# Kernel tuning notes

Measured on AMD Instinct MI355X. Metric: run time of the kernel, lower is better.

## Reference

```python
import jax, jax.numpy as jnp
import numpy as np

DIM, HEADS, K = 128, 4, 7
HD = DIM // HEADS


def _nbr_idx(n, k):
    # NATTEN boundary-clamped neighborhood (dilation=1): window start clamped to [0, n-k]
    i = np.arange(n)
    start = np.clip(i - k // 2, 0, n - k)
    idx = start[:, None] + np.arange(k)[None, :]          # (n, k) absolute neighbor index
    rel = idx - i[:, None] + (k - 1)                      # (n, k) index into 2k-1 rpb axis
    return jnp.asarray(idx), jnp.asarray(rel)


def _ln(x, w, b, eps=1e-5):
    mu = jnp.mean(x, -1, keepdims=True)
    var = jnp.var(x, -1, keepdims=True)
    return (x - mu) * jax.lax.rsqrt(var + eps) * w + b


def setup_inputs() -> dict:
    key = jax.random.key(0)
    ks = jax.random.split(key, 16)
    B, H, W, C = 1, 128, 128, DIM
    f = jax.random.normal
    inp = {
        'x': f(ks[0], (B, H, W, C), jnp.float32),
        'y': f(ks[1], (B, H, W, C), jnp.float32),
        'qv_w': f(ks[2], (2 * C, C), jnp.float32) * 0.02,
        'qv_b': jnp.zeros((2 * C,), jnp.float32),
        'k_w': f(ks[3], (C, C), jnp.float32) * 0.02,
        'k_b': jnp.zeros((C,), jnp.float32),
        'rpb': f(ks[4], (HEADS, 2 * K - 1, 2 * K - 1), jnp.float32) * 0.02,
        'proj_w': f(ks[5], (C, C), jnp.float32) * 0.02,
        'proj_b': jnp.zeros((C,), jnp.float32),
        'n1_w': jnp.ones((C,), jnp.float32),
        'n1_b': jnp.zeros((C,), jnp.float32),
        'n2_w': jnp.ones((C,), jnp.float32),
        'n2_b': jnp.zeros((C,), jnp.float32),
        'fc1_w': f(ks[6], (4 * C, C), jnp.float32) * 0.02,
        'fc1_b': jnp.zeros((4 * C,), jnp.float32),
        'fc2_w': f(ks[7], (C, 4 * C), jnp.float32) * 0.02,
        'fc2_b': jnp.zeros((C,), jnp.float32),
    }
    return inp


def _block(x, y, qv_w, qv_b, k_w, k_b, rpb, proj_w, proj_b,
           n1_w, n1_b, n2_w, n2_b, fc1_w, fc1_b, fc2_w, fc2_b):
    B, H, W, C = x.shape
    scale = HD ** -0.5
    # ---- CrossNat2D attention on norm1(x) vs y ----
    xn = _ln(x, n1_w, n1_b)
    qv = xn @ qv_w.T + qv_b                               # (B,H,W,2C)
    q = qv[..., :C].reshape(B, H, W, HEADS, HD) * scale
    v = qv[..., C:].reshape(B, H, W, HEADS, HD)
    k = (y @ k_w.T + k_b).reshape(B, H, W, HEADS, HD)

    idx_h, rel_h = _nbr_idx(H, K)
    idx_w, rel_w = _nbr_idx(W, K)
    # gather neighborhoods: (B, H, K, W, K, HEADS, HD)
    k_nbr = k[:, idx_h][:, :, :, idx_w]
    v_nbr = v[:, idx_h][:, :, :, idx_w]

    # attention logits over KxK neighborhood
    attn = jnp.einsum('bijhd,biajchd->bijhac', q, k_nbr)  # (B,H,W,heads,K,K)
    bias = rpb[:, rel_h][..., rel_w]                      # (heads,H,K,W,K)
    attn = attn + jnp.transpose(bias, (1, 3, 0, 2, 4))    # broadcast over B
    attn = jax.nn.softmax(attn.reshape(B, H, W, HEADS, K * K), axis=-1)
    attn = attn.reshape(B, H, W, HEADS, K, K)

    out = jnp.einsum('bijhac,biajchd->bijhd', attn, v_nbr).reshape(B, H, W, C)
    out = out @ proj_w.T + proj_b

    x = x + out
    # ---- MLP ----
    h = _ln(x, n2_w, n2_b) @ fc1_w.T + fc1_b
    h = jax.nn.gelu(h, approximate=False) @ fc2_w.T + fc2_b
    return x + h


def reference(x, y, qv_w, qv_b, k_w, k_b, rpb, proj_w, proj_b,
              n1_w, n1_b, n2_w, n2_b, fc1_w, fc1_b, fc2_w, fc2_b):
    return _block(x, y, qv_w, qv_b, k_w, k_b, rpb, proj_w, proj_b,
                  n1_w, n1_b, n2_w, n2_b, fc1_w, fc1_b, fc2_w, fc2_b)
```

## Files before the change

kernel.cpp:

```cpp
#include <hip/hip_runtime.h>
#include <hip/hip_bf16.h>


#define N_PIX 16384
#define C 128
#define HEADS 4
#define HD 32
#define HW 128

typedef __hip_bfloat16 bf16;
typedef __attribute__((ext_vector_type(8))) short bf16x8;
typedef __attribute__((ext_vector_type(4))) float f32x4;

union U32x4 { unsigned int u[4]; bf16x8 b; };

__device__ __forceinline__ short f2bs(float f) {
    bf16 h = __float2bfloat16(f);
    return (short)__bfloat16_as_ushort(h);
}
__device__ __forceinline__ float bs2f(short s) {
    __hip_bfloat16_raw r; r.x = (unsigned short)s;
    return __bfloat162float(__hip_bfloat16(r));
}
__device__ __forceinline__ float gelu_f(float v) {
    const float z = 1.5957691216f * (v + 0.044715f * v * v * v);
    return v / (1.f + __expf(-z));
}
__device__ __forceinline__ unsigned int pack2(float a, float b) {
    return (unsigned int)(unsigned short)f2bs(a) |
           ((unsigned int)(unsigned short)f2bs(b) << 16);
}

__global__ __launch_bounds__(256) void k_wconv(
    const float* __restrict__ qv_w, const float* __restrict__ k_w,
    const float* __restrict__ proj_w, const float* __restrict__ fc1_w,
    const float* __restrict__ fc2_w,
    short* __restrict__ wqv, short* __restrict__ wk, short* __restrict__ wproj,
    short* __restrict__ wfc1, short* __restrict__ wfc2) {
    const int i = blockIdx.x * 256 + threadIdx.x;
    if (i < 32768) wqv[i] = f2bs(qv_w[i]);
    if (i < 16384) { wk[i] = f2bs(k_w[i]); wproj[i] = f2bs(proj_w[i]); }
    if (i < 65536) { wfc1[i] = f2bs(fc1_w[i]); wfc2[i] = f2bs(fc2_w[i]); }
}

__global__ __launch_bounds__(256, 4) void k_qkv(
    const float* __restrict__ x, const float* __restrict__ y,
    const short* __restrict__ wqv, const float* __restrict__ qv_b,
    const short* __restrict__ wk, const float* __restrict__ k_b,
    const float* __restrict__ n1_w, const float* __restrict__ n1_b,
    bf16* __restrict__ qb, bf16* __restrict__ vb, bf16* __restrict__ kb) {
    __shared__ float xr[16][132];
    __shared__ short xn[16][136];
    __shared__ short yl[16][136];
    __shared__ float muA[16], riA[16];
    const int t = threadIdx.x;
    const int pix0 = (blockIdx.x & 7) * 2048 + (blockIdx.x >> 3) * 16;
    for (int e = t; e < 512; e += 256) {
        const int r = e >> 5, c4 = (e & 31) * 4;
        const float4 xv = *(const float4*)(x + (size_t)(pix0 + r) * C + c4);
        *(float4*)&xr[r][c4] = xv;
        const float4 yv = *(const float4*)(y + (size_t)(pix0 + r) * C + c4);
        uint2 yp; yp.x = pack2(yv.x, yv.y); yp.y = pack2(yv.z, yv.w);
        *(uint2*)&yl[r][c4] = yp;
    }
    __syncthreads();
    if (t < 128) {
        const int r = t >> 3, s = t & 7;
        float sm = 0.f, sq = 0.f;
        for (int i = 0; i < 16; i++) { float v = xr[r][s * 16 + i]; sm += v; sq += v * v; }
        for (int m = 1; m < 8; m <<= 1) { sm += __shfl_xor(sm, m, 64); sq += __shfl_xor(sq, m, 64); }
        if (s == 0) {
            const float mu = sm * (1.f / 128.f);
            const float var = sq * (1.f / 128.f) - mu * mu;
            muA[r] = mu; riA[r] = rsqrtf(var + 1e-5f);
        }
    }
    __syncthreads();
    for (int e = t; e < 2048; e += 256) {
        const int r = e >> 7, c = e & 127;
        xn[r][c] = f2bs((xr[r][c] - muA[r]) * riA[r] * n1_w[c] + n1_b[c]);
    }
    __syncthreads();
    const int wave = t >> 6, lane = t & 63, quad = lane >> 4, l15 = lane & 15;
    const float scale = 0.1767766952966369f;
    {
        bf16x8 aA[4];
#pragma unroll
        for (int kt = 0; kt < 4; kt++)
            aA[kt] = *(const bf16x8*)&xn[l15][kt * 32 + quad * 8];
#pragma unroll
        for (int s = 0; s < 4; s++) {
            const int n = (wave * 4 + s) * 16 + l15;
            f32x4 acc = {0.f, 0.f, 0.f, 0.f};
#pragma unroll
            for (int kt = 0; kt < 4; kt++) {
                bf16x8 b = *(const bf16x8*)&wqv[n * C + kt * 32 + quad * 8];
                acc = __builtin_amdgcn_mfma_f32_16x16x32_bf16(aA[kt], b, acc, 0, 0, 0);
            }
            const float bias = qv_b[n];
#pragma unroll
            for (int r = 0; r < 4; r++) {
                const int m = quad * 4 + r;
                const float v = acc[r] + bias;
                if (n < C) qb[(size_t)(pix0 + m) * C + n] = __float2bfloat16(v * scale);
                else       vb[(size_t)(pix0 + m) * C + (n - C)] = __float2bfloat16(v);
            }
        }
    }
    {
        bf16x8 aY[4];
#pragma unroll
        for (int kt = 0; kt < 4; kt++)
            aY[kt] = *(const bf16x8*)&yl[l15][kt * 32 + quad * 8];
        const int n0 = (wave * 2) * 16 + l15, n1 = (wave * 2 + 1) * 16 + l15;
        f32x4 a0 = {0.f, 0.f, 0.f, 0.f}, a1 = {0.f, 0.f, 0.f, 0.f};
#pragma unroll
        for (int kt = 0; kt < 4; kt++) {
            bf16x8 b0 = *(const bf16x8*)&wk[n0 * C + kt * 32 + quad * 8];
            bf16x8 b1 = *(const bf16x8*)&wk[n1 * C + kt * 32 + quad * 8];
            a0 = __builtin_amdgcn_mfma_f32_16x16x32_bf16(aY[kt], b0, a0, 0, 0, 0);
            a1 = __builtin_amdgcn_mfma_f32_16x16x32_bf16(aY[kt], b1, a1, 0, 0, 0);
        }
        const float b0s = k_b[n0], b1s = k_b[n1];
#pragma unroll
        for (int r = 0; r < 4; r++) {
            const int m = quad * 4 + r;
            kb[(size_t)(pix0 + m) * C + n0] = __float2bfloat16(a0[r] + b0s);
            kb[(size_t)(pix0 + m) * C + n1] = __float2bfloat16(a1[r] + b1s);
        }
    }
}

__global__ __launch_bounds__(256, 4) void k_fam(
    const bf16* __restrict__ qb, const bf16* __restrict__ kb,
    const bf16* __restrict__ vb, const float* __restrict__ rpb,
    const float* __restrict__ x,
    const short* __restrict__ wproj, const float* __restrict__ proj_b,
    const float* __restrict__ n2_w, const float* __restrict__ n2_b,
    const short* __restrict__ wfc1, const float* __restrict__ fc1_b,
    const short* __restrict__ wfc2, const float* __restrict__ fc2_b,
    float* __restrict__ out) {
    __shared__ short U[14784];
    __shared__ float muA[16], riA[16];
    short* const aoL = U;
    short* const x1b = U + 2176;
    short* const xnb = U + 4288;
    short* const hb  = U + 6464;
    const int t = threadIdx.x;
    const int wave = t >> 6, lane = t & 63, quad = lane >> 4, l15 = lane & 15;
    const int h = wave;
    const int tile = (blockIdx.x & 7) * 128 + (blockIdx.x >> 3);
    const int i0 = (tile >> 5) * 4, j0 = (tile & 31) * 4;
    const int rs = min(max(i0 - 3, 0), 118);
    const int cs = min(max(j0 - 3, 0), 118);
    const int pA = (i0 + (l15 >> 2)) * HW + j0 + (l15 & 3);
    const bf16x8 aQ = *(const bf16x8*)(qb + (size_t)pA * C + h * HD + quad * 8);
    const int nR0 = h * 16 + l15, nR1 = (h + 4) * 16 + l15;
    float xres0[4], xres1[4];
#pragma unroll
    for (int r = 0; r < 4; r++) {
        const int m = quad * 4 + r;
        const int p = (i0 + (m >> 2)) * HW + j0 + (m & 3);
        xres0[r] = x[(size_t)p * C + nR0];
        xres1[r] = x[(size_t)p * C + nR1];
    }
    uint4 vst[7];
#pragma unroll
    for (int it = 0; it < 7; ++it) {
        const int u = t + it * 256;
        const int r = u >> 4, seg = u & 15;
        const int sr = min(r, 99);
        const size_t g = (size_t)((rs + sr / 10) * HW + cs + sr % 10) * C + seg * 8;
        *(uint4*)&U[r * 132 + seg * 8] = *(const uint4*)(kb + g);
        vst[it] = *(const uint4*)(vb + g);
    }
    __syncthreads();
    f32x4 S[7];
#pragma unroll
    for (int nt = 0; nt < 7; nt++) {
        const bf16x8 bK = *(const bf16x8*)&U[(nt * 16 + l15) * 132 + h * HD + quad * 8];
        f32x4 z = {0.f, 0.f, 0.f, 0.f};
        S[nt] = __builtin_amdgcn_mfma_f32_16x16x32_bf16(bK, aQ, z, 0, 0, 0);
    }
    __syncthreads();
#pragma unroll
    for (int it = 0; it < 7; ++it) {
        const int u = t + it * 256;
        const int r = u >> 4, seg = u & 15;
        *(uint4*)&U[r * 132 + seg * 8] = vst[it];
    }
    const float* rpbh = rpb + h * 169;
    const int ii = i0 + (l15 >> 2), jj0_ = j0 + (l15 & 3);
    const int shi = min(max(ii - 3, 0), 121);
    const int swj = min(max(jj0_ - 3, 0), 121);
    float best = -1e30f;
#pragma unroll
    for (int nt = 0; nt < 7; nt++) {
#pragma unroll
        for (int r = 0; r < 4; r++) {
            const int nb = nt * 16 + quad * 4 + r;
            const int ai = rs + nb / 10, aj = cs + nb % 10;
            const bool valid = (nb < 100) & (ai >= shi) & (ai <= shi + 6) & (aj >= swj) & (aj <= swj + 6);
            const int ri = min(max(ai - ii + 6, 0), 12);
            const int rj = min(max(aj - jj0_ + 6, 0), 12);
            const float v = valid ? (S[nt][r] + rpbh[ri * 13 + rj]) : -1e30f;
            S[nt][r] = v;
            best = fmaxf(best, v);
        }
    }
    best = fmaxf(best, __shfl_xor(best, 16, 64));
    best = fmaxf(best, __shfl_xor(best, 32, 64));
    float s = 0.f;
#pragma unroll
    for (int nt = 0; nt < 7; nt++) {
#pragma unroll
        for (int r = 0; r < 4; r++) {
            const float e = __expf(S[nt][r] - best);
            S[nt][r] = e;
            s += e;
        }
    }
    s += __shfl_xor(s, 16, 64);
    s += __shfl_xor(s, 32, 64);
    const float smx = 1.f / s;
    unsigned int pk[14];
#pragma unroll
    for (int nt = 0; nt < 7; nt++) {
        pk[nt * 2]     = pack2(S[nt][0] * smx, S[nt][1] * smx);
        pk[nt * 2 + 1] = pack2(S[nt][2] * smx, S[nt][3] * smx);
    }
    __syncthreads();
    f32x4 O0 = {0.f, 0.f, 0.f, 0.f}, O1 = {0.f, 0.f, 0.f, 0.f};
#pragma unroll
    for (int kt = 0; kt < 3; kt++) {
        U32x4 uu;
#pragma unroll
        for (int w = 0; w < 4; w++) {
            const int qs = ((quad & 1) << 1) + (w >> 1);
            const int src = (qs << 4) | l15;
            const unsigned va = __shfl(pk[4 * kt + (w & 1)], src, 64);
            const unsigned vb2 = __shfl(pk[4 * kt + 2 + (w & 1)], src, 64);
            uu.u[w] = (quad >> 1) ? vb2 : va;
        }
        const bf16x8 aP = uu.b;
#pragma unroll
        for (int nt2 = 0; nt2 < 2; nt2++) {
            const int ch = h * HD + nt2 * 16 + l15;
            const int base = (kt * 32 + quad * 8) * 132 + ch;
            bf16x8 bV;
#pragma unroll
            for (int jj = 0; jj < 8; jj++) bV[jj] = U[base + jj * 132];
            if (nt2 == 0) O0 = __builtin_amdgcn_mfma_f32_16x16x32_bf16(aP, bV, O0, 0, 0, 0);
            else          O1 = __builtin_amdgcn_mfma_f32_16x16x32_bf16(aP, bV, O1, 0, 0, 0);
        }
    }
    {
        U32x4 uu;
#pragma unroll
        for (int w = 0; w < 4; w++) {
            const int qs = ((quad & 1) << 1) + (w >> 1);
            const int src = (qs << 4) | l15;
            const unsigned va = __shfl(pk[12 + (w & 1)], src, 64);
            uu.u[w] = (quad >> 1) ? 0u : va;
        }
        const bf16x8 aP = uu.b;
#pragma unroll
        for (int nt2 = 0; nt2 < 2; nt2++) {
            const int ch = h * HD + nt2 * 16 + l15;
            bf16x8 bV = {0, 0, 0, 0, 0, 0, 0, 0};
            if (quad < 2) {
                const int base = (96 + quad * 8) * 132 + ch;
#pragma unroll
                for (int jj = 0; jj < 8; jj++) bV[jj] = U[base + jj * 132];
            }
            if (nt2 == 0) O0 = __builtin_amdgcn_mfma_f32_16x16x32_bf16(aP, bV, O0, 0, 0, 0);
            else          O1 = __builtin_amdgcn_mfma_f32_16x16x32_bf16(aP, bV, O1, 0, 0, 0);
        }
    }
    __syncthreads();
#pragma unroll
    for (int r = 0; r < 4; r++) {
        const int m = quad * 4 + r;
        aoL[m * 136 + h * HD + l15] = f2bs(O0[r]);
        aoL[m * 136 + h * HD + 16 + l15] = f2bs(O1[r]);
    }
    __syncthreads();
    float x1f0[4], x1f1[4];
    {
        bf16x8 aO[4];
#pragma unroll
        for (int kt = 0; kt < 4; kt++)
            aO[kt] = *(const bf16x8*)&aoL[l15 * 136 + kt * 32 + quad * 8];
        f32x4 a0 = {0.f, 0.f, 0.f, 0.f}, a1 = {0.f, 0.f, 0.f, 0.f};
#pragma unroll
        for (int kt = 0; kt < 4; kt++) {
            bf16x8 b0 = *(const bf16x8*)&wproj[nR0 * C + kt * 32 + quad * 8];
            bf16x8 b1 = *(const bf16x8*)&wproj[nR1 * C + kt * 32 + quad * 8];
            a0 = __builtin_amdgcn_mfma_f32_16x16x32_bf16(aO[kt], b0, a0, 0, 0, 0);
            a1 = __builtin_amdgcn_mfma_f32_16x16x32_bf16(aO[kt], b1, a1, 0, 0, 0);
        }
        const float b0s = proj_b[nR0], b1s = proj_b[nR1];
#pragma unroll
        for (int r = 0; r < 4; r++) {
            const int m = quad * 4 + r;
            const float v0 = xres0[r] + a0[r] + b0s;
            const float v1 = xres1[r] + a1[r] + b1s;
            x1f0[r] = v0; x1f1[r] = v1;
            x1b[m * 132 + nR0] = f2bs(v0);
            x1b[m * 132 + nR1] = f2bs(v1);
        }
    }
    __syncthreads();
    if (t < 128) {
        const int r = t >> 3, s2 = t & 7;
        float sm = 0.f, sq = 0.f;
        for (int i2 = 0; i2 < 16; i2++) { float v = bs2f(x1b[r * 132 + s2 * 16 + i2]); sm += v; sq += v * v; }
        for (int m = 1; m < 8; m <<= 1) { sm += __shfl_xor(sm, m, 64); sq += __shfl_xor(sq, m, 64); }
        if (s2 == 0) {
            const float mu = sm * (1.f / 128.f);
            const float var = sq * (1.f / 128.f) - mu * mu;
            muA[r] = mu; riA[r] = rsqrtf(var + 1e-5f);
        }
    }
    __syncthreads();
    for (int e = t; e < 2048; e += 256) {
        const int r = e >> 7, c = e & 127;
        xnb[r * 136 + c] = f2bs((bs2f(x1b[r * 132 + c]) - muA[r]) * riA[r] * n2_w[c] + n2_b[c]);
    }
    __syncthreads();
    {
        bf16x8 aX[4];
#pragma unroll
        for (int kt = 0; kt < 4; kt++)
            aX[kt] = *(const bf16x8*)&xnb[l15 * 136 + kt * 32 + quad * 8];
#pragma unroll
        for (int a = 0; a < 8; a++) {
            const int n = (wave * 8 + a) * 16 + l15;
            f32x4 acc = {0.f, 0.f, 0.f, 0.f};
#pragma unroll
            for (int kt = 0; kt < 4; kt++) {
                bf16x8 bw = *(const bf16x8*)&wfc1[n * C + kt * 32 + quad * 8];
                acc = __builtin_amdgcn_mfma_f32_16x16x32_bf16(aX[kt], bw, acc, 0, 0, 0);
            }
            const float bias = fc1_b[n];
#pragma unroll
            for (int r = 0; r < 4; r++) {
                const int m = quad * 4 + r;
                hb[m * 520 + n] = f2bs(gelu_f(acc[r] + bias));
            }
        }
    }
    __syncthreads();
    {
        f32x4 a0 = {0.f, 0.f, 0.f, 0.f}, a1 = {0.f, 0.f, 0.f, 0.f};
#pragma unroll
        for (int kt = 0; kt < 16; kt++) {
            const bf16x8 aP = *(const bf16x8*)&hb[l15 * 520 + kt * 32 + quad * 8];
            bf16x8 b0 = *(const bf16x8*)&wfc2[nR0 * 512 + kt * 32 + quad * 8];
            bf16x8 b1 = *(const bf16x8*)&wfc2[nR1 * 512 + kt * 32 + quad * 8];
            a0 = __builtin_amdgcn_mfma_f32_16x16x32_bf16(aP, b0, a0, 0, 0, 0);
            a1 = __builtin_amdgcn_mfma_f32_16x16x32_bf16(aP, b1, a1, 0, 0, 0);
        }
        const float b0s = fc2_b[nR0], b1s = fc2_b[nR1];
#pragma unroll
        for (int r = 0; r < 4; r++) {
            const int m = quad * 4 + r;
            const int p = (i0 + (m >> 2)) * HW + j0 + (m & 3);
            out[(size_t)p * C + nR0] = a0[r] + b0s + x1f0[r];
            out[(size_t)p * C + nR1] = a1[r] + b1s + x1f1[r];
        }
    }
}

extern "C" void kernel_launch(void* const* d_in, const int* in_sizes, int n_in,
                              void* d_out, int out_size, void* d_ws, size_t ws_size,
                              hipStream_t stream) {
    const float* x      = (const float*)d_in[0];
    const float* y      = (const float*)d_in[1];
    const float* qv_w   = (const float*)d_in[2];
    const float* qv_b   = (const float*)d_in[3];
    const float* k_w    = (const float*)d_in[4];
    const float* k_b    = (const float*)d_in[5];
    const float* rpb    = (const float*)d_in[6];
    const float* proj_w = (const float*)d_in[7];
    const float* proj_b = (const float*)d_in[8];
    const float* n1_w   = (const float*)d_in[9];
    const float* n1_b   = (const float*)d_in[10];
    const float* n2_w   = (const float*)d_in[11];
    const float* n2_b   = (const float*)d_in[12];
    const float* fc1_w  = (const float*)d_in[13];
    const float* fc1_b  = (const float*)d_in[14];
    const float* fc2_w  = (const float*)d_in[15];
    const float* fc2_b  = (const float*)d_in[16];
    float* out = (float*)d_out;

    bf16* qb  = (bf16*)d_ws;
    bf16* vb  = qb + (size_t)N_PIX * C;
    bf16* kb  = vb + (size_t)N_PIX * C;
    short* wqv  = (short*)(kb + (size_t)N_PIX * C);
    short* wk   = wqv + 32768;
    short* wproj= wk + 16384;
    short* wfc1 = wproj + 16384;
    short* wfc2 = wfc1 + 65536;

    k_wconv<<<256, 256, 0, stream>>>(qv_w, k_w, proj_w, fc1_w, fc2_w,
                                     wqv, wk, wproj, wfc1, wfc2);
    k_qkv<<<1024, 256, 0, stream>>>(x, y, wqv, qv_b, wk, k_b, n1_w, n1_b,
                                    qb, vb, kb);
    k_fam<<<1024, 256, 0, stream>>>(qb, kb, vb, rpb, x, wproj, proj_b, n2_w, n2_b,
                                    wfc1, fc1_b, wfc2, fc2_b, out);
}
```

Measured before the change: 170.3 us.

## Double threads per block and split attention softmax across two wave groups

Both the QKV and fused attention+MLP kernels move from 256 to 512 threads per block, so each wave owns fewer output columns. In the attention kernel the neighbour tiles are split between two wave groups per head. Their partial max and sum are merged through shared memory, and the probabilities are staged in a new LDS buffer instead of being exchanged by cross-lane shuffles. This is meant to expose more parallel waves and shorten each wave's serial MFMA chain, at the cost of extra barriers, more LDS and a higher occupancy target that may limit registers.

Result: no change. 168.3 us (-1.2%).

```diff
diff --git a/kernel.cpp b/kernel.cpp
--- a/kernel.cpp
+++ b/kernel.cpp
@@ -11,8 +11,6 @@
 typedef __hip_bfloat16 bf16;
 typedef __attribute__((ext_vector_type(8))) short bf16x8;
 typedef __attribute__((ext_vector_type(4))) float f32x4;
-
-union U32x4 { unsigned int u[4]; bf16x8 b; };
 
 __device__ __forceinline__ short f2bs(float f) {
     bf16 h = __float2bfloat16(f);
@@ -43,7 +41,7 @@
     if (i < 65536) { wfc1[i] = f2bs(fc1_w[i]); wfc2[i] = f2bs(fc2_w[i]); }
 }
 
-__global__ __launch_bounds__(256, 4) void k_qkv(
+__global__ __launch_bounds__(512, 8) void k_qkv(
     const float* __restrict__ x, const float* __restrict__ y,
     const short* __restrict__ wqv, const float* __restrict__ qv_b,
     const short* __restrict__ wk, const float* __restrict__ k_b,
@@ -55,8 +53,8 @@
     __shared__ float muA[16], riA[16];
     const int t = threadIdx.x;
     const int pix0 = (blockIdx.x & 7) * 2048 + (blockIdx.x >> 3) * 16;
-    for (int e = t; e < 512; e += 256) {
-        const int r = e >> 5, c4 = (e & 31) * 4;
+    {
+        const int r = t >> 5, c4 = (t & 31) * 4;
         const float4 xv = *(const float4*)(x + (size_t)(pix0 + r) * C + c4);
         *(float4*)&xr[r][c4] = xv;
         const float4 yv = *(const float4*)(y + (size_t)(pix0 + r) * C + c4);
@@ -76,7 +74,7 @@
         }
     }
     __syncthreads();
-    for (int e = t; e < 2048; e += 256) {
+    for (int e = t; e < 2048; e += 512) {
         const int r = e >> 7, c = e & 127;
         xn[r][c] = f2bs((xr[r][c] - muA[r]) * riA[r] * n1_w[c] + n1_b[c]);
     }
@@ -88,23 +86,24 @@
 #pragma unroll
         for (int kt = 0; kt < 4; kt++)
             aA[kt] = *(const bf16x8*)&xn[l15][kt * 32 + quad * 8];
-#pragma unroll
-        for (int s = 0; s < 4; s++) {
-            const int n = (wave * 4 + s) * 16 + l15;
-            f32x4 acc = {0.f, 0.f, 0.f, 0.f};
-#pragma unroll
-            for (int kt = 0; kt < 4; kt++) {
-                bf16x8 b = *(const bf16x8*)&wqv[n * C + kt * 32 + quad * 8];
-                acc = __builtin_amdgcn_mfma_f32_16x16x32_bf16(aA[kt], b, acc, 0, 0, 0);
-            }
-            const float bias = qv_b[n];
-#pragma unroll
-            for (int r = 0; r < 4; r++) {
-                const int m = quad * 4 + r;
-                const float v = acc[r] + bias;
-                if (n < C) qb[(size_t)(pix0 + m) * C + n] = __float2bfloat16(v * scale);
-                else       vb[(size_t)(pix0 + m) * C + (n - C)] = __float2bfloat16(v);
-            }
+        const int n0 = (wave * 2) * 16 + l15, n1 = (wave * 2 + 1) * 16 + l15;
+        f32x4 a0 = {0.f, 0.f, 0.f, 0.f}, a1 = {0.f, 0.f, 0.f, 0.f};
+#pragma unroll
+        for (int kt = 0; kt < 4; kt++) {
+            bf16x8 b0 = *(const bf16x8*)&wqv[n0 * C + kt * 32 + quad * 8];
+            bf16x8 b1 = *(const bf16x8*)&wqv[n1 * C + kt * 32 + quad * 8];
+            a0 = __builtin_amdgcn_mfma_f32_16x16x32_bf16(aA[kt], b0, a0, 0, 0, 0);
+            a1 = __builtin_amdgcn_mfma_f32_16x16x32_bf16(aA[kt], b1, a1, 0, 0, 0);
+        }
+        const float b0s = qv_b[n0], b1s = qv_b[n1];
+#pragma unroll
+        for (int r = 0; r < 4; r++) {
+            const int m = quad * 4 + r;
+            const float v0 = a0[r] + b0s, v1 = a1[r] + b1s;
+            if (n0 < C) qb[(size_t)(pix0 + m) * C + n0] = __float2bfloat16(v0 * scale);
+            else        vb[(size_t)(pix0 + m) * C + (n0 - C)] = __float2bfloat16(v0);
+            if (n1 < C) qb[(size_t)(pix0 + m) * C + n1] = __float2bfloat16(v1 * scale);
+            else        vb[(size_t)(pix0 + m) * C + (n1 - C)] = __float2bfloat16(v1);
         }
     }
     {
@@ -112,26 +111,25 @@
 #pragma unroll
         for (int kt = 0; kt < 4; kt++)
             aY[kt] = *(const bf16x8*)&yl[l15][kt * 32 + quad * 8];
-        const int n0 = (wave * 2) * 16 + l15, n1 = (wave * 2 + 1) * 16 + l15;
+        const int n = wave * 16 + l15;
         f32x4 a0 = {0.f, 0.f, 0.f, 0.f}, a1 = {0.f, 0.f, 0.f, 0.f};
 #pragma unroll
-        for (int kt = 0; kt < 4; kt++) {
-            bf16x8 b0 = *(const bf16x8*)&wk[n0 * C + kt * 32 + quad * 8];
-            bf16x8 b1 = *(const bf16x8*)&wk[n1 * C + kt * 32 + quad * 8];
+        for (int kt = 0; kt < 4; kt += 2) {
+            bf16x8 b0 = *(const bf16x8*)&wk[n * C + kt * 32 + quad * 8];
+            bf16x8 b1 = *(const bf16x8*)&wk[n * C + (kt + 1) * 32 + quad * 8];
             a0 = __builtin_amdgcn_mfma_f32_16x16x32_bf16(aY[kt], b0, a0, 0, 0, 0);
-            a1 = __builtin_amdgcn_mfma_f32_16x16x32_bf16(aY[kt], b1, a1, 0, 0, 0);
-        }
-        const float b0s = k_b[n0], b1s = k_b[n1];
+            a1 = __builtin_amdgcn_mfma_f32_16x16x32_bf16(aY[kt + 1], b1, a1, 0, 0, 0);
+        }
+        const float bs = k_b[n];
 #pragma unroll
         for (int r = 0; r < 4; r++) {
             const int m = quad * 4 + r;
-            kb[(size_t)(pix0 + m) * C + n0] = __float2bfloat16(a0[r] + b0s);
-            kb[(size_t)(pix0 + m) * C + n1] = __float2bfloat16(a1[r] + b1s);
-        }
-    }
-}
-
-__global__ __launch_bounds__(256, 4) void k_fam(
+            kb[(size_t)(pix0 + m) * C + n] = __float2bfloat16(a0[r] + a1[r] + bs);
+        }
+    }
+}
+
+__global__ __launch_bounds__(512, 8) void k_fam(
     const bf16* __restrict__ qb, const bf16* __restrict__ kb,
     const bf16* __restrict__ vb, const float* __restrict__ rpb,
     const float* __restrict__ x,
@@ -141,6 +139,8 @@
     const short* __restrict__ wfc2, const float* __restrict__ fc2_b,
     float* __restrict__ out) {
     __shared__ short U[14784];
+    __shared__ short Pb[16 * 136];
+    __shared__ float pmax[2][4][16], psum[2][4][16];
     __shared__ float muA[16], riA[16];
     short* const aoL = U;
     short* const x1b = U + 2176;
@@ -148,144 +148,125 @@
     short* const hb  = U + 6464;
     const int t = threadIdx.x;
     const int wave = t >> 6, lane = t & 63, quad = lane >> 4, l15 = lane & 15;
-    const int h = wave;
+    const int h = wave & 3, s = wave >> 2;
     const int tile = (blockIdx.x & 7) * 128 + (blockIdx.x >> 3);
     const int i0 = (tile >> 5) * 4, j0 = (tile & 31) * 4;
     const int rs = min(max(i0 - 3, 0), 118);
     const int cs = min(max(j0 - 3, 0), 118);
     const int pA = (i0 + (l15 >> 2)) * HW + j0 + (l15 & 3);
     const bf16x8 aQ = *(const bf16x8*)(qb + (size_t)pA * C + h * HD + quad * 8);
-    const int nR0 = h * 16 + l15, nR1 = (h + 4) * 16 + l15;
-    float xres0[4], xres1[4];
+    const int nW = wave * 16 + l15;
+    float xres[4];
 #pragma unroll
     for (int r = 0; r < 4; r++) {
         const int m = quad * 4 + r;
         const int p = (i0 + (m >> 2)) * HW + j0 + (m & 3);
-        xres0[r] = x[(size_t)p * C + nR0];
-        xres1[r] = x[(size_t)p * C + nR1];
-    }
-    uint4 vst[7];
-#pragma unroll
-    for (int it = 0; it < 7; ++it) {
-        const int u = t + it * 256;
-        const int r = u >> 4, seg = u & 15;
-        const int sr = min(r, 99);
-        const size_t g = (size_t)((rs + sr / 10) * HW + cs + sr % 10) * C + seg * 8;
-        *(uint4*)&U[r * 132 + seg * 8] = *(const uint4*)(kb + g);
-        vst[it] = *(const uint4*)(vb + g);
-    }
-    __syncthreads();
-    f32x4 S[7];
-#pragma unroll
-    for (int nt = 0; nt < 7; nt++) {
-        const bf16x8 bK = *(const bf16x8*)&U[(nt * 16 + l15) * 132 + h * HD + quad * 8];
-        f32x4 z = {0.f, 0.f, 0.f, 0.f};
-        S[nt] = __builtin_amdgcn_mfma_f32_16x16x32_bf16(bK, aQ, z, 0, 0, 0);
-    }
-    __syncthreads();
-#pragma unroll
-    for (int it = 0; it < 7; ++it) {
-        const int u = t + it * 256;
-        const int r = u >> 4, seg = u & 15;
-        *(uint4*)&U[r * 132 + seg * 8] = vst[it];
+        xres[r] = x[(size_t)p * C + nW];
+    }
+    uint4 vst[4];
+#pragma unroll
+    for (int it = 0; it < 4; ++it) {
+        if (it < 3 || t < 256) {
+            const int u = t + it * 512;
+            const int r = u >> 4, seg = u & 15;
+            const int sr = min(r, 99);
+            const size_t g = (size_t)((rs + sr / 10) * HW + cs + sr % 10) * C + seg * 8;
+            *(uint4*)&U[r * 132 + seg * 8] = *(const uint4*)(kb + g);
+            vst[it] = *(const uint4*)(vb + g);
+        }
+    }
+    __syncthreads();
+    f32x4 S[4];
+#pragma unroll
+    for (int ntl = 0; ntl < 4; ntl++) {
+        if (s == 0 || ntl < 3) {
+            const int nt = s * 4 + ntl;
+            const bf16x8 bK = *(const bf16x8*)&U[(nt * 16 + l15) * 132 + h * HD + quad * 8];
+            f32x4 z = {0.f, 0.f, 0.f, 0.f};
+            S[ntl] = __builtin_amdgcn_mfma_f32_16x16x32_bf16(aQ, bK, z, 0, 0, 0);
+        }
+    }
+    __syncthreads();
+#pragma unroll
+    for (int it = 0; it < 4; ++it) {
+        if (it < 3 || t < 256) {
+            const int u = t + it * 512;
+            const int r = u >> 4, seg = u & 15;
+            *(uint4*)&U[r * 132 + seg * 8] = vst[it];
+        }
     }
     const float* rpbh = rpb + h * 169;
-    const int ii = i0 + (l15 >> 2), jj0_ = j0 + (l15 & 3);
-    const int shi = min(max(ii - 3, 0), 121);
-    const int swj = min(max(jj0_ - 3, 0), 121);
-    float best = -1e30f;
-#pragma unroll
-    for (int nt = 0; nt < 7; nt++) {
-#pragma unroll
-        for (int r = 0; r < 4; r++) {
-            const int nb = nt * 16 + quad * 4 + r;
-            const int ai = rs + nb / 10, aj = cs + nb % 10;
-            const bool valid = (nb < 100) & (ai >= shi) & (ai <= shi + 6) & (aj >= swj) & (aj <= swj + 6);
-            const int ri = min(max(ai - ii + 6, 0), 12);
-            const int rj = min(max(aj - jj0_ + 6, 0), 12);
-            const float v = valid ? (S[nt][r] + rpbh[ri * 13 + rj]) : -1e30f;
-            S[nt][r] = v;
-            best = fmaxf(best, v);
-        }
-    }
-    best = fmaxf(best, __shfl_xor(best, 16, 64));
-    best = fmaxf(best, __shfl_xor(best, 32, 64));
-    float s = 0.f;
-#pragma unroll
-    for (int nt = 0; nt < 7; nt++) {
-#pragma unroll
-        for (int r = 0; r < 4; r++) {
-            const float e = __expf(S[nt][r] - best);
-            S[nt][r] = e;
-            s += e;
-        }
-    }
-    s += __shfl_xor(s, 16, 64);
-    s += __shfl_xor(s, 32, 64);
-    const float smx = 1.f / s;
-    unsigned int pk[14];
-#pragma unroll
-    for (int nt = 0; nt < 7; nt++) {
-        pk[nt * 2]     = pack2(S[nt][0] * smx, S[nt][1] * smx);
-        pk[nt * 2 + 1] = pack2(S[nt][2] * smx, S[nt][3] * smx);
-    }
-    __syncthreads();
-    f32x4 O0 = {0.f, 0.f, 0.f, 0.f}, O1 = {0.f, 0.f, 0.f, 0.f};
-#pragma unroll
-    for (int kt = 0; kt < 3; kt++) {
-        U32x4 uu;
-#pragma unroll
-        for (int w = 0; w < 4; w++) {
-            const int qs = ((quad & 1) << 1) + (w >> 1);
-            const int src = (qs << 4) | l15;
-            const unsigned va = __shfl(pk[4 * kt + (w & 1)], src, 64);
-            const unsigned vb2 = __shfl(pk[4 * kt + 2 + (w & 1)], src, 64);
-            uu.u[w] = (quad >> 1) ? vb2 : va;
-        }
-        const bf16x8 aP = uu.b;
-#pragma unroll
-        for (int nt2 = 0; nt2 < 2; nt2++) {
-            const int ch = h * HD + nt2 * 16 + l15;
-            const int base = (kt * 32 + quad * 8) * 132 + ch;
-            bf16x8 bV;
-#pragma unroll
-            for (int jj = 0; jj < 8; jj++) bV[jj] = U[base + jj * 132];
-            if (nt2 == 0) O0 = __builtin_amdgcn_mfma_f32_16x16x32_bf16(aP, bV, O0, 0, 0, 0);
-            else          O1 = __builtin_amdgcn_mfma_f32_16x16x32_bf16(aP, bV, O1, 0, 0, 0);
-        }
-    }
-    {
-        U32x4 uu;
-#pragma unroll
-        for (int w = 0; w < 4; w++) {
-            const int qs = ((quad & 1) << 1) + (w >> 1);
-            const int src = (qs << 4) | l15;
-            const unsigned va = __shfl(pk[12 + (w & 1)], src, 64);
-            uu.u[w] = (quad >> 1) ? 0u : va;
-        }
-        const bf16x8 aP = uu.b;
-#pragma unroll
-        for (int nt2 = 0; nt2 < 2; nt2++) {
-            const int ch = h * HD + nt2 * 16 + l15;
-            bf16x8 bV = {0, 0, 0, 0, 0, 0, 0, 0};
-            if (quad < 2) {
-                const int base = (96 + quad * 8) * 132 + ch;
-#pragma unroll
-                for (int jj = 0; jj < 8; jj++) bV[jj] = U[base + jj * 132];
-            }
-            if (nt2 == 0) O0 = __builtin_amdgcn_mfma_f32_16x16x32_bf16(aP, bV, O0, 0, 0, 0);
-            else          O1 = __builtin_amdgcn_mfma_f32_16x16x32_bf16(aP, bV, O1, 0, 0, 0);
-        }
-    }
-    __syncthreads();
+    float mo[4];
 #pragma unroll
     for (int r = 0; r < 4; r++) {
         const int m = quad * 4 + r;
-        aoL[m * 136 + h * HD + l15] = f2bs(O0[r]);
-        aoL[m * 136 + h * HD + 16 + l15] = f2bs(O1[r]);
-    }
-    __syncthreads();
-    float x1f0[4], x1f1[4];
+        const int ii = i0 + (m >> 2), jj = j0 + (m & 3);
+        const int shi = min(max(ii - 3, 0), 121);
+        const int swj = min(max(jj - 3, 0), 121);
+        float best = -1e30f;
+#pragma unroll
+        for (int ntl = 0; ntl < 4; ntl++) {
+            if (s == 0 || ntl < 3) {
+                const int nb = (s * 4 + ntl) * 16 + l15;
+                const int ai = rs + nb / 10, aj = cs + nb % 10;
+                const bool valid = (nb < 100) & (ai >= shi) & (ai <= shi + 6) & (aj >= swj) & (aj <= swj + 6);
+                const int ri = min(max(ai - ii + 6, 0), 12);
+                const int rj = min(max(aj - jj + 6, 0), 12);
+                const float v = valid ? (S[ntl][r] + rpbh[ri * 13 + rj]) : -1e30f;
+                S[ntl][r] = v;
+                best = fmaxf(best, v);
+            }
+        }
+        for (int msk = 1; msk < 16; msk <<= 1) best = fmaxf(best, __shfl_xor(best, msk, 64));
+        mo[r] = best;
+        float sum = 0.f;
+#pragma unroll
+        for (int ntl = 0; ntl < 4; ntl++) {
+            if (s == 0 || ntl < 3) {
+                const float e = __expf(S[ntl][r] - best);
+                S[ntl][r] = e;
+                sum += e;
+            }
+        }
+        for (int msk = 1; msk < 16; msk <<= 1) sum += __shfl_xor(sum, msk, 64);
+        if (l15 == 0) { pmax[s][h][m] = best; psum[s][h][m] = sum; }
+    }
+    __syncthreads();
+#pragma unroll
+    for (int r = 0; r < 4; r++) {
+        const int m = quad * 4 + r;
+        const float m0 = pmax[0][h][m], m1 = pmax[1][h][m];
+        const float s0 = psum[0][h][m], s1 = psum[1][h][m];
+        const float mf = fmaxf(m0, m1);
+        const float Sf = s0 * __expf(m0 - mf) + s1 * __expf(m1 - mf);
+        const float sc = __expf(mo[r] - mf) / Sf;
+#pragma unroll
+        for (int ntl = 0; ntl < 4; ntl++) {
+            if (s == 0 || ntl < 3)
+                Pb[m * 136 + (s * 4 + ntl) * 16 + l15] = f2bs(S[ntl][r] * sc);
+        }
+    }
+    __syncthreads();
+    f32x4 O = {0.f, 0.f, 0.f, 0.f};
+    const int ch = h * HD + s * 16 + l15;
+#pragma unroll
+    for (int kt = 0; kt < 4; kt++) {
+        bf16x8 aP = {0, 0, 0, 0, 0, 0, 0, 0};
+        bf16x8 bV = {0, 0, 0, 0, 0, 0, 0, 0};
+        if (kt < 3 || quad < 2) {
+            aP = *(const bf16x8*)&Pb[l15 * 136 + kt * 32 + quad * 8];
+            const int base = (kt * 32 + quad * 8) * 132 + ch;
+#pragma unroll
+            for (int jj = 0; jj < 8; jj++) bV[jj] = U[base + jj * 132];
+        }
+        O = __builtin_amdgcn_mfma_f32_16x16x32_bf16(aP, bV, O, 0, 0, 0);
+    }
+    __syncthreads();
+#pragma unroll
+    for (int r = 0; r < 4; r++)
+        aoL[(quad * 4 + r) * 136 + ch] = f2bs(O[r]);
+    __syncthreads();
+    float x1f[4];
     {
         bf16x8 aO[4];
 #pragma unroll
@@ -293,21 +274,19 @@
             aO[kt] = *(const bf16x8*)&aoL[l15 * 136 + kt * 32 + quad * 8];
         f32x4 a0 = {0.f, 0.f, 0.f, 0.f}, a1 = {0.f, 0.f, 0.f, 0.f};
 #pragma unroll
-        for (int kt = 0; kt < 4; kt++) {
-            bf16x8 b0 = *(const bf16x8*)&wproj[nR0 * C + kt * 32 + quad * 8];
-            bf16x8 b1 = *(const bf16x8*)&wproj[nR1 * C + kt * 32 + quad * 8];
+        for (int kt = 0; kt < 4; kt += 2) {
+            bf16x8 b0 = *(const bf16x8*)&wproj[nW * C + kt * 32 + quad * 8];
+            bf16x8 b1 = *(const bf16x8*)&wproj[nW * C + (kt + 1) * 32 + quad * 8];
             a0 = __builtin_amdgcn_mfma_f32_16x16x32_bf16(aO[kt], b0, a0, 0, 0, 0);
-            a1 = __builtin_amdgcn_mfma_f32_16x16x32_bf16(aO[kt], b1, a1, 0, 0, 0);
-        }
-        const float b0s = proj_b[nR0], b1s = proj_b[nR1];
+            a1 = __builtin_amdgcn_mfma_f32_16x16x32_bf16(aO[kt + 1], b1, a1, 0, 0, 0);
+        }
+        const float bs = proj_b[nW];
 #pragma unroll
         for (int r = 0; r < 4; r++) {
             const int m = quad * 4 + r;
-            const float v0 = xres0[r] + a0[r] + b0s;
-            const float v1 = xres1[r] + a1[r] + b1s;
-            x1f0[r] = v0; x1f1[r] = v1;
-            x1b[m * 132 + nR0] = f2bs(v0);
-            x1b[m * 132 + nR1] = f2bs(v1);
+            const float v = xres[r] + a0[r] + a1[r] + bs;
+            x1f[r] = v;
+            x1b[m * 132 + nW] = f2bs(v);
         }
     }
     __syncthreads();
@@ -323,7 +302,7 @@
         }
     }
     __syncthreads();
-    for (int e = t; e < 2048; e += 256) {
+    for (int e = t; e < 2048; e += 512) {
         const int r = e >> 7, c = e & 127;
         xnb[r * 136 + c] = f2bs((bs2f(x1b[r * 132 + c]) - muA[r]) * riA[r] * n2_w[c] + n2_b[c]);
     }
@@ -334,8 +313,8 @@
         for (int kt = 0; kt < 4; kt++)
             aX[kt] = *(const bf16x8*)&xnb[l15 * 136 + kt * 32 + quad * 8];
 #pragma unroll
-        for (int a = 0; a < 8; a++) {
-            const int n = (wave * 8 + a) * 16 + l15;
+        for (int a = 0; a < 4; a++) {
+            const int n = (wave * 4 + a) * 16 + l15;
             f32x4 acc = {0.f, 0.f, 0.f, 0.f};
 #pragma unroll
             for (int kt = 0; kt < 4; kt++) {
@@ -354,20 +333,20 @@
     {
         f32x4 a0 = {0.f, 0.f, 0.f, 0.f}, a1 = {0.f, 0.f, 0.f, 0.f};
 #pragma unroll
-        for (int kt = 0; kt < 16; kt++) {
-            const bf16x8 aP = *(const bf16x8*)&hb[l15 * 520 + kt * 32 + quad * 8];
-            bf16x8 b0 = *(const bf16x8*)&wfc2[nR0 * 512 + kt * 32 + quad * 8];
-            bf16x8 b1 = *(const bf16x8*)&wfc2[nR1 * 512 + kt * 32 + quad * 8];
-            a0 = __builtin_amdgcn_mfma_f32_16x16x32_bf16(aP, b0, a0, 0, 0, 0);
-            a1 = __builtin_amdgcn_mfma_f32_16x16x32_bf16(aP, b1, a1, 0, 0, 0);
-        }
-        const float b0s = fc2_b[nR0], b1s = fc2_b[nR1];
+        for (int kt = 0; kt < 16; kt += 2) {
+            const bf16x8 aPe = *(const bf16x8*)&hb[l15 * 520 + kt * 32 + quad * 8];
+            const bf16x8 aPo = *(const bf16x8*)&hb[l15 * 520 + (kt + 1) * 32 + quad * 8];
+            bf16x8 b0 = *(const bf16x8*)&wfc2[nW * 512 + kt * 32 + quad * 8];
+            bf16x8 b1 = *(const bf16x8*)&wfc2[nW * 512 + (kt + 1) * 32 + quad * 8];
+            a0 = __builtin_amdgcn_mfma_f32_16x16x32_bf16(aPe, b0, a0, 0, 0, 0);
+            a1 = __builtin_amdgcn_mfma_f32_16x16x32_bf16(aPo, b1, a1, 0, 0, 0);
+        }
+        const float bs = fc2_b[nW];
 #pragma unroll
         for (int r = 0; r < 4; r++) {
             const int m = quad * 4 + r;
             const int p = (i0 + (m >> 2)) * HW + j0 + (m & 3);
-            out[(size_t)p * C + nR0] = a0[r] + b0s + x1f0[r];
-            out[(size_t)p * C + nR1] = a1[r] + b1s + x1f1[r];
+            out[(size_t)p * C + nW] = a0[r] + a1[r] + bs + x1f[r];
         }
     }
 }
@@ -405,8 +384,8 @@
 
     k_wconv<<<256, 256, 0, stream>>>(qv_w, k_w, proj_w, fc1_w, fc2_w,
                                      wqv, wk, wproj, wfc1, wfc2);
-    k_qkv<<<1024, 256, 0, stream>>>(x, y, wqv, qv_b, wk, k_b, n1_w, n1_b,
+    k_qkv<<<1024, 512, 0, stream>>>(x, y, wqv, qv_b, wk, k_b, n1_w, n1_b,
                                     qb, vb, kb);
-    k_fam<<<1024, 256, 0, stream>>>(qb, kb, vb, rpb, x, wproj, proj_b, n2_w, n2_b,
+    k_fam<<<1024, 512, 0, stream>>>(qb, kb, vb, rpb, x, wproj, proj_b, n2_w, n2_b,
                                     wfc1, fc1_b, wfc2, fc2_b, out);
 }
```
